# Optimization experiments

Measured on AMD Instinct MI355X. Metric: run time of the kernel, lower is better.

## Reference

```python
import jax, jax.numpy as jnp
import numpy as np
from math import sqrt

B, T, DMODEL = 4, 2048, 512
N_HEADS, DK, DV = 8, 64, 64
FF_INNER = 2048


def setup_inputs() -> dict:
    key = jax.random.key(0)
    ks = jax.random.split(key, 10)
    u = lambda k, shape: jax.random.uniform(k, shape, jnp.float32, -1.0, 1.0)
    x = jax.random.normal(ks[0], (B, T, DMODEL), jnp.float32)
    Wq = u(ks[1], (N_HEADS, DMODEL, DK))
    Wk = u(ks[2], (N_HEADS, DMODEL, DK))
    Wv = u(ks[3], (N_HEADS, DMODEL, DV))
    Wo = u(ks[4], (N_HEADS * DV, DMODEL))
    # FeedForward: Linear(dmodel->inner) then Linear(inner->dmodel); stored as (in, out)
    lim1 = 1.0 / sqrt(DMODEL)
    lim2 = 1.0 / sqrt(FF_INNER)
    W1 = jax.random.uniform(ks[5], (DMODEL, FF_INNER), jnp.float32, -lim1, lim1)
    b1 = jax.random.uniform(ks[6], (FF_INNER,), jnp.float32, -lim1, lim1)
    W2 = jax.random.uniform(ks[7], (FF_INNER, DMODEL), jnp.float32, -lim2, lim2)
    b2 = jax.random.uniform(ks[8], (DMODEL,), jnp.float32, -lim2, lim2)
    return {"x": x, "Wq": Wq, "Wk": Wk, "Wv": Wv, "Wo": Wo,
            "W1": W1, "b1": b1, "W2": W2, "b2": b2}


def reference(x, Wq, Wk, Wv, Wo, W1, b1, W2, b2):
    Bx, Tx = x.shape[0], x.shape[1]
    # per-head projections: (B,1,T,dmodel) @ (H,dmodel,dk) -> (B,H,T,dk)
    q = jnp.einsum('btd,hdk->bhtk', x, Wq)
    k = jnp.einsum('btd,hdk->bhtk', x, Wk)
    v = jnp.einsum('btd,hdv->bhtv', x, Wv)
    scale = 1.0 / sqrt(DK)
    scores = jnp.einsum('bhtk,bhsk->bhts', q, k) * scale  # (B,H,T,T)
    attn = jax.nn.softmax(scores, axis=-1)
    att = jnp.einsum('bhts,bhsv->bhtv', attn, v)  # (B,H,T,dv)
    # faithful to the original: raw reshape (B,H,T,dv)->(B,T,H*dv), no head transpose
    att = att.reshape(Bx, Tx, N_HEADS * DV)
    out = att @ Wo  # (B,T,dmodel)
    # FeedForward: Linear -> ReLU -> Linear
    h = jax.nn.relu(out @ W1 + b1)
    return h @ W2 + b2
```

## Files before the change

### kernel.cpp

```cpp
#include <hip/hip_runtime.h>
#include <hip/hip_bf16.h>

typedef short bf16x8 __attribute__((ext_vector_type(8)));
typedef float f32x4 __attribute__((ext_vector_type(4)));

#define MFMA_BF16(A,B,C) __builtin_amdgcn_mfma_f32_16x16x32_bf16((A),(B),(C),0,0,0)

__device__ __forceinline__ unsigned short f2bf(float f){
    union { float f; unsigned u; } v; v.f = f;
    unsigned r = v.u + 0x7fffu + ((v.u >> 16) & 1u);
    return (unsigned short)(r >> 16);
}
__device__ __forceinline__ float bf2f(unsigned short h){
    union { unsigned u; float f; } v; v.u = ((unsigned)h) << 16; return v.f;
}

__global__ __launch_bounds__(256) void k_cvt_split(const float* __restrict__ in,
                                                   unsigned short* __restrict__ hi,
                                                   unsigned short* __restrict__ lo, int n){
    int i = blockIdx.x * 256 + threadIdx.x;
    if (i < n) {
        float v = in[i];
        unsigned short h = f2bf(v);
        hi[i] = h;
        lo[i] = f2bf(v - bf2f(h));
    }
}

__global__ __launch_bounds__(256) void k_prep_qkT(const float* __restrict__ Wq,
                                                  const float* __restrict__ Wk,
                                                  unsigned short* __restrict__ hi,
                                                  unsigned short* __restrict__ lo){
    int idx = blockIdx.x * 256 + threadIdx.x;
    int c = idx >> 9, d = idx & 511;
    int t = c >> 9, rem = c & 511;
    int h = rem >> 6, k = rem & 63;
    const float* W = (t == 0) ? Wq : Wk;
    float v = W[(h * 512 + d) * 64 + k];
    unsigned short hh = f2bf(v);
    hi[idx] = hh;
    lo[idx] = f2bf(v - bf2f(hh));
}

__global__ __launch_bounds__(256) void k_prep_wvT(const float* __restrict__ Wv,
                                                  unsigned short* __restrict__ out){
    int idx = blockIdx.x * 256 + threadIdx.x;
    int row = idx >> 9, d = idx & 511;
    int h = row >> 6, k = row & 63;
    out[idx] = f2bf(Wv[(h * 512 + d) * 64 + k]);
}

__global__ __launch_bounds__(256) void k_prep_T(const float* __restrict__ W,
                                                unsigned short* __restrict__ out, int D, int N){
    int idx = blockIdx.x * 256 + threadIdx.x;
    int n = idx / D, d = idx - n * D;
    out[idx] = f2bf(W[d * N + n]);
}

template<int EPI, bool SPLIT>
__global__ __launch_bounds__(256)
void gemm_bt(const unsigned short* __restrict__ Ah, const unsigned short* __restrict__ Al,
             const unsigned short* __restrict__ Bh, const unsigned short* __restrict__ Bl,
             int M, int N, int K, const float* __restrict__ bias,
             unsigned short* __restrict__ Cb, float* __restrict__ Cf,
             unsigned short* __restrict__ Qh, unsigned short* __restrict__ Ql,
             unsigned short* __restrict__ Kh, unsigned short* __restrict__ Kl,
             unsigned short* __restrict__ Vo)
{
    constexpr int BK = 32, LDP = 40;
    constexpr int NS = SPLIT ? 2 : 1;
    __shared__ __align__(16) unsigned short As[NS][128][LDP];
    __shared__ __align__(16) unsigned short Bs[NS][128][LDP];

    const int tid = threadIdx.x, lane = tid & 63, wave = tid >> 6;
    const int wr = wave >> 1, wc = wave & 1;
    const int bm = blockIdx.y, bn = blockIdx.x;
    const int rA0 = bm * 128, cB0 = bn * 128;
    const int fr = lane & 15, fg = lane >> 4;

    f32x4 acc[4][4];
    #pragma unroll
    for (int m = 0; m < 4; m++)
        #pragma unroll
        for (int n = 0; n < 4; n++)
            acc[m][n] = f32x4{0.f, 0.f, 0.f, 0.f};

    for (int kt = 0; kt < K; kt += BK) {
        __syncthreads();
        #pragma unroll
        for (int q = 0; q < 2; q++) {
            int ch = tid + q * 256;
            int r = ch >> 2, kk = (ch & 3) << 3;
            size_t ga = (size_t)(rA0 + r) * K + kt + kk;
            size_t gb = (size_t)(cB0 + r) * K + kt + kk;
            *(uint4*)&As[0][r][kk] = *(const uint4*)&Ah[ga];
            *(uint4*)&Bs[0][r][kk] = *(const uint4*)&Bh[gb];
            if constexpr (SPLIT) {
                *(uint4*)&As[1][r][kk] = *(const uint4*)&Al[ga];
                *(uint4*)&Bs[1][r][kk] = *(const uint4*)&Bl[gb];
            }
        }
        __syncthreads();

        bf16x8 afh[4], bfh[4], afl[4], bfl[4];
        #pragma unroll
        for (int m = 0; m < 4; m++) afh[m] = *(const bf16x8*)&As[0][wr * 64 + m * 16 + fr][fg * 8];
        #pragma unroll
        for (int n = 0; n < 4; n++) bfh[n] = *(const bf16x8*)&Bs[0][wc * 64 + n * 16 + fr][fg * 8];
        if constexpr (SPLIT) {
            #pragma unroll
            for (int m = 0; m < 4; m++) afl[m] = *(const bf16x8*)&As[1][wr * 64 + m * 16 + fr][fg * 8];
            #pragma unroll
            for (int n = 0; n < 4; n++) bfl[n] = *(const bf16x8*)&Bs[1][wc * 64 + n * 16 + fr][fg * 8];
        }
        #pragma unroll
        for (int m = 0; m < 4; m++)
            #pragma unroll
            for (int n = 0; n < 4; n++) {
                acc[m][n] = MFMA_BF16(afh[m], bfh[n], acc[m][n]);
                if constexpr (SPLIT) {
                    acc[m][n] = MFMA_BF16(afl[m], bfh[n], acc[m][n]);
                    acc[m][n] = MFMA_BF16(afh[m], bfl[n], acc[m][n]);
                }
            }
    }

    #pragma unroll
    for (int m = 0; m < 4; m++) {
        #pragma unroll
        for (int n = 0; n < 4; n++) {
            #pragma unroll
            for (int j = 0; j < 4; j++) {
                int row = rA0 + wr * 64 + m * 16 + fg * 4 + j;
                int col = cB0 + wc * 64 + n * 16 + fr;
                float v = acc[m][n][j];
                if constexpr (EPI == 1 || EPI == 2) v += bias[col];
                if constexpr (EPI == 1) v = fmaxf(v, 0.f);
                if constexpr (EPI == 0 || EPI == 1) {
                    Cb[(size_t)row * N + col] = f2bf(v);
                } else if constexpr (EPI == 2) {
                    Cf[(size_t)row * N + col] = v;
                } else if constexpr (EPI == 3) {
                    int t = col >> 9, h = (col >> 6) & 7, k = col & 63;
                    int b = row >> 11, tt = row & 2047;
                    size_t di = ((size_t)((b << 3) + h) * 2048 + tt) * 64 + k;
                    unsigned short hh = f2bf(v);
                    if (t == 0) { Qh[di] = hh; Ql[di] = f2bf(v - bf2f(hh)); }
                    else        { Kh[di] = hh; Kl[di] = f2bf(v - bf2f(hh)); }
                } else {
                    int h = row >> 6, k = row & 63;
                    int b = col >> 11, tt = col & 2047;
                    Vo[(((size_t)(b * 8 + h) * 64 + k) << 11) + tt] = f2bf(v);
                }
            }
        }
    }
}

__global__ __launch_bounds__(256)
void attn_kernel(const unsigned short* __restrict__ Qh, const unsigned short* __restrict__ Ql,
                 const unsigned short* __restrict__ Kh, const unsigned short* __restrict__ Kl,
                 const unsigned short* __restrict__ Vt, unsigned short* __restrict__ Ob)
{
    constexpr int T = 2048;
    __shared__ __align__(16) unsigned short Ksh[64][72];
    __shared__ __align__(16) unsigned short Ksl[64][72];
    __shared__ __align__(16) unsigned short Vts[64 * 64];
    __shared__ __align__(16) unsigned short Plds[4][16][72];

    const int tid = threadIdx.x, lane = tid & 63, wave = tid >> 6;
    const int bh = blockIdx.x >> 5;
    const int q0 = (blockIdx.x & 31) * 64;
    const size_t base = (size_t)bh * T * 64;
    const int fr = lane & 15, fg = lane >> 4;

    const size_t qoff = base + (size_t)(q0 + wave * 16 + fr) * 64;
    bf16x8 aq0h = *(const bf16x8*)&Qh[qoff + fg * 8];
    bf16x8 aq1h = *(const bf16x8*)&Qh[qoff + 32 + fg * 8];
    bf16x8 aq0l = *(const bf16x8*)&Ql[qoff + fg * 8];
    bf16x8 aq1l = *(const bf16x8*)&Ql[qoff + 32 + fg * 8];

    f32x4 o[4];
    #pragma unroll
    for (int n = 0; n < 4; n++) o[n] = f32x4{0.f, 0.f, 0.f, 0.f};
    float mrun[4] = {-1e30f, -1e30f, -1e30f, -1e30f};
    float lrun[4] = {0.f, 0.f, 0.f, 0.f};

    const int srow = tid >> 3, c8 = (tid & 7) << 3;
    char* vbase = (char*)Vts;

    for (int s0 = 0; s0 < T; s0 += 64) {
        __syncthreads();
        #pragma unroll
        for (int it = 0; it < 2; it++) {
            int r = srow + it * 32;
            size_t g = base + (size_t)(s0 + r) * 64 + c8;
            *(uint4*)&Ksh[r][c8] = *(const uint4*)&Kh[g];
            *(uint4*)&Ksl[r][c8] = *(const uint4*)&Kl[g];
            uint4 vv = *(const uint4*)&Vt[((size_t)(bh * 64 + r) << 11) + s0 + c8];
            int byteoff = r * 128 + ((c8 * 2) ^ ((r & 7) << 4));
            *(uint4*)(vbase + byteoff) = vv;
        }
        __syncthreads();

        f32x4 sc[4];
        #pragma unroll
        for (int c = 0; c < 4; c++) {
            bf16x8 b0h = *(const bf16x8*)&Ksh[c * 16 + fr][fg * 8];
            bf16x8 b1h = *(const bf16x8*)&Ksh[c * 16 + fr][32 + fg * 8];
            bf16x8 b0l = *(const bf16x8*)&Ksl[c * 16 + fr][fg * 8];
            bf16x8 b1l = *(const bf16x8*)&Ksl[c * 16 + fr][32 + fg * 8];
            f32x4 z = f32x4{0.f, 0.f, 0.f, 0.f};
            z = MFMA_BF16(aq0h, b0h, z);
            z = MFMA_BF16(aq0l, b0h, z);
            z = MFMA_BF16(aq0h, b0l, z);
            z = MFMA_BF16(aq1h, b1h, z);
            z = MFMA_BF16(aq1l, b1h, z);
            z = MFMA_BF16(aq1h, b1l, z);
            sc[c] = z * 0.125f;
        }

        float alpha[4];
        #pragma unroll
        for (int r = 0; r < 4; r++) {
            float v = fmaxf(fmaxf(sc[0][r], sc[1][r]), fmaxf(sc[2][r], sc[3][r]));
            v = fmaxf(v, __shfl_xor(v, 1)); v = fmaxf(v, __shfl_xor(v, 2));
            v = fmaxf(v, __shfl_xor(v, 4)); v = fmaxf(v, __shfl_xor(v, 8));
            float mn = fmaxf(mrun[r], v);
            alpha[r] = __expf(mrun[r] - mn);
            mrun[r] = mn;
        }
        float rs[4] = {0.f, 0.f, 0.f, 0.f};
        #pragma unroll
        for (int c = 0; c < 4; c++)
            #pragma unroll
            for (int r = 0; r < 4; r++) {
                float p = __expf(sc[c][r] - mrun[r]);
                sc[c][r] = p;
                rs[r] += p;
            }
        #pragma unroll
        for (int r = 0; r < 4; r++) {
            float t = rs[r];
            t += __shfl_xor(t, 1); t += __shfl_xor(t, 2);
            t += __shfl_xor(t, 4); t += __shfl_xor(t, 8);
            lrun[r] = lrun[r] * alpha[r] + t;
            #pragma unroll
            for (int n = 0; n < 4; n++) o[n][r] *= alpha[r];
        }

        #pragma unroll
        for (int c = 0; c < 4; c++)
            #pragma unroll
            for (int r = 0; r < 4; r++)
                Plds[wave][fg * 4 + r][c * 16 + fr] = f2bf(sc[c][r]);
        __syncthreads();

        bf16x8 pa0 = *(const bf16x8*)&Plds[wave][fr][fg * 8];
        bf16x8 pa1 = *(const bf16x8*)&Plds[wave][fr][32 + fg * 8];
        #pragma unroll
        for (int n = 0; n < 4; n++) {
            int row = n * 16 + fr;
            bf16x8 bv0 = *(const bf16x8*)(vbase + row * 128 + ((fg * 16)      ^ ((row & 7) << 4)));
            bf16x8 bv1 = *(const bf16x8*)(vbase + row * 128 + ((64 + fg * 16) ^ ((row & 7) << 4)));
            o[n] = MFMA_BF16(pa0, bv0, o[n]);
            o[n] = MFMA_BF16(pa1, bv1, o[n]);
        }
    }

    #pragma unroll
    for (int r = 0; r < 4; r++) {
        float inv = 1.0f / lrun[r];
        #pragma unroll
        for (int n = 0; n < 4; n++) o[n][r] *= inv;
    }
    #pragma unroll
    for (int n = 0; n < 4; n++)
        #pragma unroll
        for (int r = 0; r < 4; r++)
            Ob[base + (size_t)(q0 + wave * 16 + fg * 4 + r) * 64 + n * 16 + fr] = f2bf(o[n][r]);
}

extern "C" void kernel_launch(void* const* d_in, const int* in_sizes, int n_in,
                              void* d_out, int out_size, void* d_ws, size_t ws_size,
                              hipStream_t stream)
{
    const float* x  = (const float*)d_in[0];
    const float* Wq = (const float*)d_in[1];
    const float* Wk = (const float*)d_in[2];
    const float* Wv = (const float*)d_in[3];
    const float* Wo = (const float*)d_in[4];
    const float* W1 = (const float*)d_in[5];
    const float* b1 = (const float*)d_in[6];
    const float* W2 = (const float*)d_in[7];
    const float* b2 = (const float*)d_in[8];
    float* out = (float*)d_out;

    char* ws = (char*)d_ws;
    size_t off = 0;
    auto alloc = [&](size_t bytes) -> void* {
        void* p = ws + off; off += (bytes + 255) & ~(size_t)255; return p;
    };
    unsigned short* wqkTh = (unsigned short*)alloc(1024ull * 512 * 2);
    unsigned short* wqkTl = (unsigned short*)alloc(1024ull * 512 * 2);
    unsigned short* wvT   = (unsigned short*)alloc(512ull * 512 * 2);
    unsigned short* woT   = (unsigned short*)alloc(512ull * 512 * 2);
    unsigned short* w1T   = (unsigned short*)alloc(2048ull * 512 * 2);
    unsigned short* w2T   = (unsigned short*)alloc(512ull * 2048 * 2);
    unsigned short* Qhb   = (unsigned short*)alloc(8192ull * 512 * 2);
    unsigned short* Qlb   = (unsigned short*)alloc(8192ull * 512 * 2);
    unsigned short* Khb   = (unsigned short*)alloc(8192ull * 512 * 2);
    unsigned short* Klb   = (unsigned short*)alloc(8192ull * 512 * 2);
    unsigned short* Vtb   = (unsigned short*)alloc(8192ull * 512 * 2);
    unsigned short* xh    = (unsigned short*)alloc(8192ull * 512 * 2);
    unsigned short* xl    = (unsigned short*)alloc(8192ull * 512 * 2);
    unsigned short* attb = xh;
    unsigned short* outb = xl;
    unsigned short* hb   = Qhb;

    k_cvt_split<<<8192 * 512 / 256, 256, 0, stream>>>(x, xh, xl, 8192 * 512);
    k_prep_qkT<<<1024 * 512 / 256, 256, 0, stream>>>(Wq, Wk, wqkTh, wqkTl);
    k_prep_wvT<<<512 * 512 / 256, 256, 0, stream>>>(Wv, wvT);
    k_prep_T<<<512 * 512 / 256, 256, 0, stream>>>(Wo, woT, 512, 512);
    k_prep_T<<<2048 * 512 / 256, 256, 0, stream>>>(W1, w1T, 512, 2048);
    k_prep_T<<<512 * 2048 / 256, 256, 0, stream>>>(W2, w2T, 2048, 512);

    gemm_bt<3, true><<<dim3(1024 / 128, 8192 / 128), 256, 0, stream>>>(
        xh, xl, wqkTh, wqkTl, 8192, 1024, 512, nullptr,
        nullptr, nullptr, Qhb, Qlb, Khb, Klb, nullptr);

    gemm_bt<4, false><<<dim3(8192 / 128, 512 / 128), 256, 0, stream>>>(
        wvT, nullptr, xh, nullptr, 512, 8192, 512, nullptr,
        nullptr, nullptr, nullptr, nullptr, nullptr, nullptr, Vtb);

    attn_kernel<<<4 * 8 * (2048 / 64), 256, 0, stream>>>(Qhb, Qlb, Khb, Klb, Vtb, attb);

    gemm_bt<0, false><<<dim3(512 / 128, 8192 / 128), 256, 0, stream>>>(
        attb, nullptr, woT, nullptr, 8192, 512, 512, nullptr,
        outb, nullptr, nullptr, nullptr, nullptr, nullptr, nullptr);

    gemm_bt<1, false><<<dim3(2048 / 128, 8192 / 128), 256, 0, stream>>>(
        outb, nullptr, w1T, nullptr, 8192, 2048, 512, b1,
        hb, nullptr, nullptr, nullptr, nullptr, nullptr, nullptr);

    gemm_bt<2, false><<<dim3(512 / 128, 8192 / 128), 256, 0, stream>>>(
        hb, nullptr, w2T, nullptr, 8192, 512, 2048, b2,
        nullptr, out, nullptr, nullptr, nullptr, nullptr, nullptr);
}
```

Baseline: 404.9 us.

## Use direct global-to-LDS loads in GEMM and tiled transposes for weight prep

The GEMM tile loads now go straight from global memory into LDS with global_load_lds, bypassing registers, and the padded LDS rows are removed so the layout matches the load order. The weight transpose and convert kernels are replaced by one shared-memory tiled transpose kernel, and the x split-conversion is vectorised to float4. This targets register round-trips during tile staging and uncoalesced strided reads in the prep kernels. Dropping the LDS padding may add bank conflicts on the MFMA fragment reads.

```diff
diff --git a/kernel.cpp b/kernel.cpp
--- a/kernel.cpp
+++ b/kernel.cpp
@@ -15,46 +15,48 @@
     union { unsigned u; float f; } v; v.u = ((unsigned)h) << 16; return v.f;
 }
 
-__global__ __launch_bounds__(256) void k_cvt_split(const float* __restrict__ in,
-                                                   unsigned short* __restrict__ hi,
-                                                   unsigned short* __restrict__ lo, int n){
+__device__ __forceinline__ void gl_lds16(const unsigned short* g, void* l){
+    __builtin_amdgcn_global_load_lds(
+        (const __attribute__((address_space(1))) unsigned int*)g,
+        (__attribute__((address_space(3))) unsigned int*)l, 16, 0, 0);
+}
+
+__global__ __launch_bounds__(256) void k_cvt_split(const float4* __restrict__ in,
+                                                   ushort4* __restrict__ hi,
+                                                   ushort4* __restrict__ lo, int n4){
     int i = blockIdx.x * 256 + threadIdx.x;
-    if (i < n) {
-        float v = in[i];
-        unsigned short h = f2bf(v);
-        hi[i] = h;
-        lo[i] = f2bf(v - bf2f(h));
-    }
-}
-
-__global__ __launch_bounds__(256) void k_prep_qkT(const float* __restrict__ Wq,
-                                                  const float* __restrict__ Wk,
-                                                  unsigned short* __restrict__ hi,
-                                                  unsigned short* __restrict__ lo){
-    int idx = blockIdx.x * 256 + threadIdx.x;
-    int c = idx >> 9, d = idx & 511;
-    int t = c >> 9, rem = c & 511;
-    int h = rem >> 6, k = rem & 63;
-    const float* W = (t == 0) ? Wq : Wk;
-    float v = W[(h * 512 + d) * 64 + k];
-    unsigned short hh = f2bf(v);
-    hi[idx] = hh;
-    lo[idx] = f2bf(v - bf2f(hh));
-}
-
-__global__ __launch_bounds__(256) void k_prep_wvT(const float* __restrict__ Wv,
-                                                  unsigned short* __restrict__ out){
-    int idx = blockIdx.x * 256 + threadIdx.x;
-    int row = idx >> 9, d = idx & 511;
-    int h = row >> 6, k = row & 63;
-    out[idx] = f2bf(Wv[(h * 512 + d) * 64 + k]);
-}
-
-__global__ __launch_bounds__(256) void k_prep_T(const float* __restrict__ W,
-                                                unsigned short* __restrict__ out, int D, int N){
-    int idx = blockIdx.x * 256 + threadIdx.x;
-    int n = idx / D, d = idx - n * D;
-    out[idx] = f2bf(W[d * N + n]);
+    if (i < n4) {
+        float4 v = in[i];
+        ushort4 h, l;
+        h.x = f2bf(v.x); l.x = f2bf(v.x - bf2f(h.x));
+        h.y = f2bf(v.y); l.y = f2bf(v.y - bf2f(h.y));
+        h.z = f2bf(v.z); l.z = f2bf(v.z - bf2f(h.z));
+        h.w = f2bf(v.w); l.w = f2bf(v.w - bf2f(h.w));
+        hi[i] = h; lo[i] = l;
+    }
+}
+
+__global__ __launch_bounds__(256)
+void k_transT(const float* __restrict__ in, long inHeadStride,
+              unsigned short* __restrict__ hi, unsigned short* __restrict__ lo,
+              int R, int C, long outBase){
+    __shared__ float t[32][33];
+    const float* src = in + (size_t)blockIdx.z * inHeadStride;
+    int c0 = blockIdx.x * 32, r0 = blockIdx.y * 32;
+    int tx = threadIdx.x & 31, ty = threadIdx.x >> 5;
+    #pragma unroll
+    for (int i = 0; i < 4; i++)
+        t[ty + i * 8][tx] = src[(size_t)(r0 + ty + i * 8) * C + c0 + tx];
+    __syncthreads();
+    size_t ob = (size_t)outBase + (size_t)blockIdx.z * C * R;
+    #pragma unroll
+    for (int i = 0; i < 4; i++) {
+        int c = c0 + ty + i * 8, r = r0 + tx;
+        float v = t[tx][ty + i * 8];
+        unsigned short hh = f2bf(v);
+        hi[ob + (size_t)c * R + r] = hh;
+        if (lo) lo[ob + (size_t)c * R + r] = f2bf(v - bf2f(hh));
+    }
 }
 
 template<int EPI, bool SPLIT>
@@ -67,15 +69,14 @@
              unsigned short* __restrict__ Kh, unsigned short* __restrict__ Kl,
              unsigned short* __restrict__ Vo)
 {
-    constexpr int BK = 32, LDP = 40;
+    constexpr int BK = 32;
     constexpr int NS = SPLIT ? 2 : 1;
-    __shared__ __align__(16) unsigned short As[NS][128][LDP];
-    __shared__ __align__(16) unsigned short Bs[NS][128][LDP];
+    __shared__ __align__(16) unsigned short As[NS][128][BK];
+    __shared__ __align__(16) unsigned short Bs[NS][128][BK];
 
     const int tid = threadIdx.x, lane = tid & 63, wave = tid >> 6;
     const int wr = wave >> 1, wc = wave & 1;
-    const int bm = blockIdx.y, bn = blockIdx.x;
-    const int rA0 = bm * 128, cB0 = bn * 128;
+    const int rA0 = blockIdx.y * 128, cB0 = blockIdx.x * 128;
     const int fr = lane & 15, fg = lane >> 4;
 
     f32x4 acc[4][4];
@@ -89,15 +90,19 @@
         __syncthreads();
         #pragma unroll
         for (int q = 0; q < 2; q++) {
-            int ch = tid + q * 256;
+            int ch = q * 256 + tid;
             int r = ch >> 2, kk = (ch & 3) << 3;
             size_t ga = (size_t)(rA0 + r) * K + kt + kk;
             size_t gb = (size_t)(cB0 + r) * K + kt + kk;
-            *(uint4*)&As[0][r][kk] = *(const uint4*)&Ah[ga];
-            *(uint4*)&Bs[0][r][kk] = *(const uint4*)&Bh[gb];
+            char* la0 = (char*)&As[0][0][0] + (q * 256 + wave * 64) * 16;
+            char* lb0 = (char*)&Bs[0][0][0] + (q * 256 + wave * 64) * 16;
+            gl_lds16(&Ah[ga], la0);
+            gl_lds16(&Bh[gb], lb0);
             if constexpr (SPLIT) {
-                *(uint4*)&As[1][r][kk] = *(const uint4*)&Al[ga];
-                *(uint4*)&Bs[1][r][kk] = *(const uint4*)&Bl[gb];
+                char* la1 = (char*)&As[1][0][0] + (q * 256 + wave * 64) * 16;
+                char* lb1 = (char*)&Bs[1][0][0] + (q * 256 + wave * 64) * 16;
+                gl_lds16(&Al[ga], la1);
+                gl_lds16(&Bl[gb], lb1);
             }
         }
         __syncthreads();
@@ -318,12 +323,14 @@
     unsigned short* outb = xl;
     unsigned short* hb   = Qhb;
 
-    k_cvt_split<<<8192 * 512 / 256, 256, 0, stream>>>(x, xh, xl, 8192 * 512);
-    k_prep_qkT<<<1024 * 512 / 256, 256, 0, stream>>>(Wq, Wk, wqkTh, wqkTl);
-    k_prep_wvT<<<512 * 512 / 256, 256, 0, stream>>>(Wv, wvT);
-    k_prep_T<<<512 * 512 / 256, 256, 0, stream>>>(Wo, woT, 512, 512);
-    k_prep_T<<<2048 * 512 / 256, 256, 0, stream>>>(W1, w1T, 512, 2048);
-    k_prep_T<<<512 * 2048 / 256, 256, 0, stream>>>(W2, w2T, 2048, 512);
+    k_cvt_split<<<8192 * 512 / 4 / 256, 256, 0, stream>>>(
+        (const float4*)x, (ushort4*)xh, (ushort4*)xl, 8192 * 512 / 4);
+    k_transT<<<dim3(2, 16, 8), 256, 0, stream>>>(Wq, 512 * 64, wqkTh, wqkTl, 512, 64, 0);
+    k_transT<<<dim3(2, 16, 8), 256, 0, stream>>>(Wk, 512 * 64, wqkTh, wqkTl, 512, 64, 512 * 512);
+    k_transT<<<dim3(2, 16, 8), 256, 0, stream>>>(Wv, 512 * 64, wvT, nullptr, 512, 64, 0);
+    k_transT<<<dim3(16, 16, 1), 256, 0, stream>>>(Wo, 0, woT, nullptr, 512, 512, 0);
+    k_transT<<<dim3(64, 16, 1), 256, 0, stream>>>(W1, 0, w1T, nullptr, 512, 2048, 0);
+    k_transT<<<dim3(16, 64, 1), 256, 0, stream>>>(W2, 0, w2T, nullptr, 2048, 512, 0);
 
     gemm_bt<3, true><<<dim3(1024 / 128, 8192 / 128), 256, 0, stream>>>(
         xh, xl, wqkTh, wqkTl, 8192, 1024, 512, nullptr,
```

Result: faster. 388.8 us (-4.0%).
